# Optimization experiments

Hardware: AMD Instinct MI355X
Metric: run time of the kernel (lower is better)

The kernel has to match this reference:

```python
import jax, jax.numpy as jnp
import numpy as np

N_NODES = 50000
N_EDGES = 800000
IN, HID, OUT = 512, 256, 128


def spmm(edge_src, edge_dst, edge_weight, x, n_nodes):
    # y[i] = sum_{e: dst[e]==i} w[e] * x[src[e]]   (sparse adjacency @ x)
    msgs = edge_weight[:, None] * x[edge_src]          # [E, F] gather
    return jax.ops.segment_sum(msgs, edge_dst, num_segments=n_nodes)


def setup_inputs() -> dict:
    key = jax.random.key(0)
    k1, k2, k3, k4, k5, k6 = jax.random.split(key, 6)
    features = jax.random.normal(k1, (N_NODES, IN), dtype=jnp.float32)
    edge_src = jax.random.randint(k2, (N_EDGES,), 0, N_NODES, dtype=jnp.int32)
    edge_dst = jax.random.randint(k3, (N_EDGES,), 0, N_NODES, dtype=jnp.int32)
    edge_weight = jax.random.uniform(k4, (N_EDGES,), dtype=jnp.float32)
    # init like torch: uniform(-stdv, stdv), stdv = 1/sqrt(out_dim)
    s1 = 1.0 / np.sqrt(HID)
    s2 = 1.0 / np.sqrt(OUT)
    W1 = jax.random.uniform(k5, (IN, HID), dtype=jnp.float32, minval=-s1, maxval=s1)
    W2 = jax.random.uniform(k6, (HID, OUT), dtype=jnp.float32, minval=-s2, maxval=s2)
    return {"features": features, "edge_src": edge_src, "edge_dst": edge_dst,
            "edge_weight": edge_weight, "W1": W1, "W2": W2}


def reference(features, edge_src, edge_dst, edge_weight, W1, W2):
    n = features.shape[0]
    # layer 1: dense GEMM -> SpMM -> ReLU
    hidden = jax.nn.relu(spmm(edge_src, edge_dst, edge_weight, features @ W1, n))
    # layer 2: dense GEMM -> SpMM
    out = spmm(edge_src, edge_dst, edge_weight, hidden @ W2, n)
    return out
```

## Files before the change

kernel.cpp:

```cpp
#include <hip/hip_runtime.h>

#define NN 50000
#define NE 800000
#define FIN 512
#define FHID 256
#define FOUT 128
#define MPAD 50048

#define TW1_BLOCKS  512
#define TW2_BLOCKS  128
#define ZERO_BLOCKS 13

#define NBKT   196
#define BCAP   5120
#define BSTRIDE 16
#define PA_BLOCKS 392
#define E_CHA    2048

#define PB_BLOCKS   196
#define GEMM1_BLOCKS 782

using bf16x8 = __attribute__((ext_vector_type(8))) short;
using f32x4  = __attribute__((ext_vector_type(4))) float;
using u16x8  = __attribute__((ext_vector_type(8))) unsigned short;
using u16x4  = __attribute__((ext_vector_type(4))) unsigned short;
using u16x2  = __attribute__((ext_vector_type(2))) unsigned short;

__device__ __forceinline__ unsigned short f2bf(float f) {
    unsigned int u = __builtin_bit_cast(unsigned int, f);
    unsigned int r = (u + 0x7FFFu + ((u >> 16) & 1u)) >> 16;
    return (unsigned short)r;
}
__device__ __forceinline__ float bf2f(unsigned short u) {
    return __builtin_bit_cast(float, (unsigned int)u << 16);
}
__device__ __forceinline__ void gload_lds16(const void* g, void* l) {
    __builtin_amdgcn_global_load_lds(
        (const __attribute__((address_space(1))) void*)g,
        (__attribute__((address_space(3))) void*)l, 16, 0, 0);
}


__global__ __launch_bounds__(256) void prep_kernel(
    int* __restrict__ bcur,
    const float* __restrict__ W1, unsigned short* __restrict__ W1T,
    const float* __restrict__ W2, unsigned short* __restrict__ W2T) {
    int b = blockIdx.x, tid = threadIdx.x;
    if (b < TW1_BLOCKS) {
        int t = b * 256 + tid;
        int n = t % FHID, k = t / FHID;
        W1T[(size_t)n * FIN + k] = f2bf(W1[t]);
    } else if (b < TW1_BLOCKS + TW2_BLOCKS) {
        int t = (b - TW1_BLOCKS) * 256 + tid;
        int n = t % FOUT, k = t / FOUT;
        W2T[(size_t)n * FHID + k] = f2bf(W2[t]);
    } else {
        int i = (b - TW1_BLOCKS - TW2_BLOCKS) * 256 + tid;
        if (i < NBKT * BSTRIDE) bcur[i] = 0;
    }
}


__global__ __launch_bounds__(256) void passa_kernel(const int* __restrict__ src,
                                                    const int* __restrict__ dst,
                                                    const float* __restrict__ w,
                                                    int* __restrict__ bcur,
                                                    int2* __restrict__ barr) {
    __shared__ int hist[NBKT];
    __shared__ int resv[NBKT];
    int pa = blockIdx.x, tid = threadIdx.x;
    if (tid < NBKT) hist[tid] = 0;
    __syncthreads();
    int base = pa * E_CHA + tid;
    int  d[8];
    bool m[8];
#pragma unroll
    for (int j = 0; j < 8; ++j) {
        int e = base + j * 256;
        m[j] = e < NE;
        d[j] = m[j] ? dst[e] : 0;
    }
#pragma unroll
    for (int j = 0; j < 8; ++j)
        if (m[j]) atomicAdd(&hist[d[j] >> 8], 1);
    __syncthreads();
    if (tid < NBKT) {
        int h = hist[tid];
        resv[tid] = (h > 0) ? atomicAdd(&bcur[tid * BSTRIDE], h) : 0;
        hist[tid] = 0;
    }
    __syncthreads();
    int   s[8];
    float wv[8];
#pragma unroll
    for (int j = 0; j < 8; ++j) {
        int e = base + j * 256;
        s[j]  = m[j] ? src[e] : 0;
        wv[j] = m[j] ? w[e] : 0.f;
    }
#pragma unroll
    for (int j = 0; j < 8; ++j) {
        if (m[j]) {
            int bb = d[j] >> 8;
            int r  = atomicAdd(&hist[bb], 1);
            int pos = resv[bb] + r;
            if (pos < BCAP)
                barr[(size_t)bb * BCAP + pos] =
                    make_int2(s[j] | ((d[j] & 255) << 16), __float_as_int(wv[j]));
        }
    }
}


__global__ __launch_bounds__(256) void scan_bkt_kernel(const int* __restrict__ bcur,
                                                       int* __restrict__ bko,
                                                       int* __restrict__ off) {
    __shared__ int wsum[4];
    int tid = threadIdx.x, lane = tid & 63, wid = tid >> 6;
    int v = (tid < NBKT) ? min(bcur[tid * BSTRIDE], BCAP) : 0;
    int s = v;
#pragma unroll
    for (int d = 1; d < 64; d <<= 1) {
        int t = __shfl_up(s, d, 64);
        if (lane >= d) s += t;
    }
    if (lane == 63) wsum[wid] = s;
    __syncthreads();
    int wo = 0;
#pragma unroll
    for (int j = 0; j < 4; ++j)
        if (j < wid) wo += wsum[j];
    int excl = wo + s - v;
    if (tid < NBKT) bko[tid] = excl;
    if (tid == NBKT - 1) off[NN] = excl + v;
}


__device__ __forceinline__ void gemm1_body(const float* __restrict__ X,
                                           const unsigned short* __restrict__ BT,
                                           unsigned short* __restrict__ C,
                                           int bx, int by) {
    __shared__ unsigned short As[128 * 64];
    __shared__ unsigned short Bs[128 * 64];

    const int tid  = threadIdx.x;
    const int lane = tid & 63;
    const int wid  = tid >> 6;
    const int wm   = wid >> 1;
    const int wn   = wid & 1;
    const int brow = bx * 128;
    const int bcol = by * 128;
    const int r15   = lane & 15;
    const int khalf = (lane >> 4) * 8;

    f32x4 acc[4][4] = {};

    for (int k0 = 0; k0 < FIN; k0 += 64) {
#pragma unroll
        for (int c = 0; c < 4; ++c) {
            int b   = wid * 4096 + c * 1024 + lane * 16;
            int row = b >> 7;
            int cby = (b & 127) ^ ((row & 7) << 4);
            const char* gb = (const char*)(BT + (size_t)(bcol + row) * FIN + k0) + cby;
            gload_lds16(gb, (char*)Bs + wid * 4096 + c * 1024);
        }
#pragma unroll
        for (int g = 0; g < 4; ++g) {
            int idx  = g * 256 + tid;
            int row  = idx >> 3;
            int col0 = (idx & 7) * 8;
            float4 a0 = make_float4(0.f, 0.f, 0.f, 0.f), a1 = a0;
            int grow = brow + row;
            if (grow < NN) {
                const float4* p = (const float4*)(X + (size_t)grow * FIN + k0 + col0);
                a0 = p[0]; a1 = p[1];
            }
            u16x8 v;
            v[0] = f2bf(a0.x); v[1] = f2bf(a0.y); v[2] = f2bf(a0.z); v[3] = f2bf(a0.w);
            v[4] = f2bf(a1.x); v[5] = f2bf(a1.y); v[6] = f2bf(a1.z); v[7] = f2bf(a1.w);
            int byte = row * 128 + ((col0 * 2) ^ ((row & 7) << 4));
            *(u16x8*)((char*)As + byte) = v;
        }
        __syncthreads();

        bf16x8 af[4][2], bfr[4][2];
#pragma unroll
        for (int m = 0; m < 4; ++m) {
            int row = wm * 64 + m * 16 + r15;
            int rb  = row * 128;
            int sw  = (row & 7) << 4;
#pragma unroll
            for (int ks = 0; ks < 2; ++ks) {
                int byte = rb + (((ks * 32 + khalf) * 2) ^ sw);
                af[m][ks] = *(const bf16x8*)((const char*)As + byte);
            }
        }
#pragma unroll
        for (int n = 0; n < 4; ++n) {
            int row = wn * 64 + n * 16 + r15;
            int rb  = row * 128;
            int sw  = (row & 7) << 4;
#pragma unroll
            for (int ks = 0; ks < 2; ++ks) {
                int byte = rb + (((ks * 32 + khalf) * 2) ^ sw);
                bfr[n][ks] = *(const bf16x8*)((const char*)Bs + byte);
            }
        }
#pragma unroll
        for (int m = 0; m < 4; ++m)
#pragma unroll
            for (int n = 0; n < 4; ++n)
#pragma unroll
                for (int ks = 0; ks < 2; ++ks)
                    acc[m][n] = __builtin_amdgcn_mfma_f32_16x16x32_bf16(
                        af[m][ks], bfr[n][ks], acc[m][n], 0, 0, 0);
        __syncthreads();
    }

    const int crow0 = brow + wm * 64;
    const int ccol0 = bcol + wn * 64 + r15;
    const int rsub  = (lane >> 4) * 4;
#pragma unroll
    for (int m = 0; m < 4; ++m) {
#pragma unroll
        for (int r = 0; r < 4; ++r) {
            int grow = crow0 + m * 16 + rsub + r;
            if (grow < NN) {
#pragma unroll
                for (int n = 0; n < 4; ++n)
                    C[(size_t)grow * FHID + ccol0 + n * 16] = f2bf(acc[m][n][r]);
            }
        }
    }
}


template <int K, int N>
__device__ __forceinline__ void gemm_body(const unsigned short* __restrict__ A,
                                          const unsigned short* __restrict__ BT,
                                          unsigned short* __restrict__ C,
                                          int M, int bx, int by) {
    __shared__ unsigned short As[128 * 64];
    __shared__ unsigned short Bs[128 * 64];

    const int tid  = threadIdx.x;
    const int lane = tid & 63;
    const int wid  = tid >> 6;
    const int wm   = wid >> 1;
    const int wn   = wid & 1;
    const int brow = bx * 128;
    const int bcol = by * 128;
    const int r15   = lane & 15;
    const int khalf = (lane >> 4) * 8;

    f32x4 acc[4][4] = {};

    for (int k0 = 0; k0 < K; k0 += 64) {
#pragma unroll
        for (int c = 0; c < 4; ++c) {
            int b   = wid * 4096 + c * 1024 + lane * 16;
            int row = b >> 7;
            int cby = (b & 127) ^ ((row & 7) << 4);
            const char* ga = (const char*)(A + (size_t)(brow + row) * K + k0) + cby;
            gload_lds16(ga, (char*)As + wid * 4096 + c * 1024);
            const char* gb = (const char*)(BT + (size_t)(bcol + row) * K + k0) + cby;
            gload_lds16(gb, (char*)Bs + wid * 4096 + c * 1024);
        }
        __syncthreads();

        bf16x8 af[4][2], bfr[4][2];
#pragma unroll
        for (int m = 0; m < 4; ++m) {
            int row = wm * 64 + m * 16 + r15;
            int rb  = row * 128;
            int sw  = (row & 7) << 4;
#pragma unroll
            for (int ks = 0; ks < 2; ++ks) {
                int byte = rb + (((ks * 32 + khalf) * 2) ^ sw);
                af[m][ks] = *(const bf16x8*)((const char*)As + byte);
            }
        }
#pragma unroll
        for (int n = 0; n < 4; ++n) {
            int row = wn * 64 + n * 16 + r15;
            int rb  = row * 128;
            int sw  = (row & 7) << 4;
#pragma unroll
            for (int ks = 0; ks < 2; ++ks) {
                int byte = rb + (((ks * 32 + khalf) * 2) ^ sw);
                bfr[n][ks] = *(const bf16x8*)((const char*)Bs + byte);
            }
        }
#pragma unroll
        for (int m = 0; m < 4; ++m)
#pragma unroll
            for (int n = 0; n < 4; ++n)
#pragma unroll
                for (int ks = 0; ks < 2; ++ks)
                    acc[m][n] = __builtin_amdgcn_mfma_f32_16x16x32_bf16(
                        af[m][ks], bfr[n][ks], acc[m][n], 0, 0, 0);
        __syncthreads();
    }

    const int crow0 = brow + wm * 64;
    const int ccol0 = bcol + wn * 64 + r15;
    const int rsub  = (lane >> 4) * 4;
#pragma unroll
    for (int m = 0; m < 4; ++m) {
#pragma unroll
        for (int r = 0; r < 4; ++r) {
            int grow = crow0 + m * 16 + rsub + r;
            if (grow < M) {
#pragma unroll
                for (int n = 0; n < 4; ++n)
                    C[(size_t)grow * N + ccol0 + n * 16] = f2bf(acc[m][n][r]);
            }
        }
    }
}


__device__ __forceinline__ void passb_body(int b, const int2* __restrict__ barr,
                                           const int* __restrict__ bcur,
                                           const int* __restrict__ bko,
                                           int* __restrict__ off,
                                           int2* __restrict__ csr) {
    __shared__ int cnt[256];
    __shared__ int pre[256];
    __shared__ int wsum[4];
    int tid = threadIdx.x, lane = tid & 63, wid = tid >> 6;
    int total = min(bcur[b * BSTRIDE], BCAP);
    int bko_b = bko[b];
    const int2* seg = barr + (size_t)b * BCAP;

    cnt[tid] = 0;
    __syncthreads();
    for (int k = tid; k < total; k += 256)
        atomicAdd(&cnt[(seg[k].x >> 16) & 255], 1);
    __syncthreads();
    int v = cnt[tid];
    int s = v;
#pragma unroll
    for (int d = 1; d < 64; d <<= 1) {
        int t = __shfl_up(s, d, 64);
        if (lane >= d) s += t;
    }
    if (lane == 63) wsum[wid] = s;
    __syncthreads();
    int wo = 0;
#pragma unroll
    for (int j = 0; j < 4; ++j)
        if (j < wid) wo += wsum[j];
    int base = bko_b + wo + s - v;
    pre[tid] = base;
    int n = b * 256 + tid;
    if (n < NN) off[n] = base;
    cnt[tid] = 0;
    __syncthreads();
    for (int k = tid; k < total; k += 256) {
        int2 pl = seg[k];
        int dlow = (pl.x >> 16) & 255;
        int r = atomicAdd(&cnt[dlow], 1);
        csr[pre[dlow] + r] = make_int2(pl.x & 0xFFFF, pl.y);
    }
}


__global__ __launch_bounds__(256) void fused_gemm1_finalize_kernel(
    const float* __restrict__ X, const unsigned short* __restrict__ BT,
    unsigned short* __restrict__ C,
    const int2* __restrict__ barr, const int* __restrict__ bcur,
    const int* __restrict__ bko, int* __restrict__ off, int2* __restrict__ csr) {
    if (blockIdx.x < PB_BLOCKS) {
        passb_body(blockIdx.x, barr, bcur, bko, off, csr);
    } else {
        int g = blockIdx.x - PB_BLOCKS;
        gemm1_body(X, BT, C, g % 391, g / 391);
    }
}

template <int K, int N>
__global__ __launch_bounds__(256) void gemm_bf16_kernel(const unsigned short* __restrict__ A,
                                                        const unsigned short* __restrict__ BT,
                                                        unsigned short* __restrict__ C,
                                                        int M) {
    gemm_body<K, N>(A, BT, C, M, blockIdx.x, blockIdx.y);
}


__global__ __launch_bounds__(256) void spmm_pair_kernel(const unsigned short* __restrict__ X,
                                                        const int* __restrict__ off,
                                                        const int2* __restrict__ csr,
                                                        unsigned short* __restrict__ Y) {
    int wave = (int)((blockIdx.x * 256 + threadIdx.x) >> 6);
    int lane = threadIdx.x & 63;
    int half = lane >> 5;
    int hl   = lane & 31;
    int n = wave * 2 + half;
    if (n >= NN) return;
    int e0 = off[n];
    int e1 = off[n + 1];
    const size_t fo = (size_t)hl * 8;

    float acc[8] = {};
    for (int e = e0; e < e1; e += 8) {
        int   ss[8];
        float ww[8];
#pragma unroll
        for (int j = 0; j < 8; ++j) {
            int  ee = e + j;
            bool v  = ee < e1;
            int2 sw = csr[v ? ee : e0];
            ss[j] = sw.x;
            ww[j] = v ? __int_as_float(sw.y) : 0.f;
        }
        u16x8 r[8];
#pragma unroll
        for (int j = 0; j < 8; ++j)
            r[j] = *(const u16x8*)(X + (size_t)ss[j] * FHID + fo);
#pragma unroll
        for (int j = 0; j < 8; ++j)
#pragma unroll
            for (int k = 0; k < 8; ++k)
                acc[k] += ww[j] * bf2f(r[j][k]);
    }
    u16x8 o;
#pragma unroll
    for (int k = 0; k < 8; ++k) o[k] = f2bf(fmaxf(acc[k], 0.f));
    *(u16x8*)(Y + (size_t)n * FHID + fo) = o;
}


__global__ __launch_bounds__(256) void spmm_quad_kernel(const unsigned short* __restrict__ X,
                                                        const int* __restrict__ off,
                                                        const int2* __restrict__ csr,
                                                        float* __restrict__ Y) {
    int wave = (int)((blockIdx.x * 256 + threadIdx.x) >> 6);
    int lane = threadIdx.x & 63;
    int q  = lane >> 4;
    int hl = lane & 15;
    int n = wave * 4 + q;
    if (n >= NN) return;
    int e0 = off[n];
    int e1 = off[n + 1];
    const size_t fo = (size_t)hl * 8;

    float acc[8] = {};
    for (int e = e0; e < e1; e += 8) {
        int   ss[8];
        float ww[8];
#pragma unroll
        for (int j = 0; j < 8; ++j) {
            int  ee = e + j;
            bool v  = ee < e1;
            int2 sw = csr[v ? ee : e0];
            ss[j] = sw.x;
            ww[j] = v ? __int_as_float(sw.y) : 0.f;
        }
        u16x8 r[8];
#pragma unroll
        for (int j = 0; j < 8; ++j)
            r[j] = *(const u16x8*)(X + (size_t)ss[j] * FOUT + fo);
#pragma unroll
        for (int j = 0; j < 8; ++j)
#pragma unroll
            for (int k = 0; k < 8; ++k)
                acc[k] += ww[j] * bf2f(r[j][k]);
    }
    float4 o0 = make_float4(acc[0], acc[1], acc[2], acc[3]);
    float4 o1 = make_float4(acc[4], acc[5], acc[6], acc[7]);
    *(float4*)(Y + (size_t)n * FOUT + fo) = o0;
    *(float4*)(Y + (size_t)n * FOUT + fo + 4) = o1;
}


extern "C" void kernel_launch(void* const* d_in, const int* in_sizes, int n_in,
                              void* d_out, int out_size, void* d_ws, size_t ws_size,
                              hipStream_t stream) {
    const float* features = (const float*)d_in[0];
    const int*   edge_src = (const int*)d_in[1];
    const int*   edge_dst = (const int*)d_in[2];
    const float* edge_w   = (const float*)d_in[3];
    const float* W1       = (const float*)d_in[4];
    const float* W2       = (const float*)d_in[5];
    float* out = (float*)d_out;

    char*  ws  = (char*)d_ws;
    size_t ofs = 0;
    auto carve = [&](size_t bytes) -> void* {
        void* r = ws + ofs;
        ofs = (ofs + bytes + 255) & ~(size_t)255;
        return r;
    };
    int*            off   = (int*)carve((NN + 1) * sizeof(int));
    int*            bcur  = (int*)carve(NBKT * BSTRIDE * sizeof(int));
    int*            bko   = (int*)carve(NBKT * sizeof(int));
    int2*           barr  = (int2*)carve((size_t)NBKT * BCAP * sizeof(int2));
    int2*           csr   = (int2*)carve((size_t)NE * sizeof(int2));
    unsigned short* W1T   = (unsigned short*)carve((size_t)FHID * FIN * 2);
    unsigned short* W2T   = (unsigned short*)carve((size_t)FOUT * FHID * 2);
    unsigned short* H0b   = (unsigned short*)carve((size_t)MPAD * FHID * 2);
    unsigned short* Hb    = (unsigned short*)carve((size_t)MPAD * FHID * 2);
    unsigned short* H1b   = H0b;

    prep_kernel<<<TW1_BLOCKS + TW2_BLOCKS + ZERO_BLOCKS, 256, 0, stream>>>(
        bcur, W1, W1T, W2, W2T);

    passa_kernel<<<PA_BLOCKS, 256, 0, stream>>>(edge_src, edge_dst, edge_w, bcur, barr);

    scan_bkt_kernel<<<1, 256, 0, stream>>>(bcur, bko, off);

    fused_gemm1_finalize_kernel<<<PB_BLOCKS + GEMM1_BLOCKS, 256, 0, stream>>>(
        features, W1T, H0b, barr, bcur, bko, off, csr);

    spmm_pair_kernel<<<6250, 256, 0, stream>>>(H0b, off, csr, Hb);

    gemm_bf16_kernel<FHID, FOUT><<<dim3(391, 1), 256, 0, stream>>>(Hb, W2T, H1b, NN);
    spmm_quad_kernel<<<3125, 256, 0, stream>>>(H1b, off, csr, out);
}
```

Before: 175.4 us.

## Fuse pass A bucketing with GEMM1, fold bucket scan into pass B, shrink GEMM tiles

The pipeline is reordered so the edge-bucketing pass runs in the same launch as the first dense GEMM, and the CSR finalize pass becomes its own kernel that recomputes the bucket prefix scan in every block. The separate single-block scan kernel is removed. Both GEMMs move from 128-row to 64-row tiles, doubling the block count to improve occupancy and load balance. In exchange, the large GEMM1 no longer overlaps with pass B, and the smaller tiles lower per-block data reuse.

```diff
diff --git a/kernel.cpp b/kernel.cpp
--- a/kernel.cpp
+++ b/kernel.cpp
@@ -17,14 +17,14 @@
 #define PA_BLOCKS 392
 #define E_CHA    2048
 
-#define PB_BLOCKS   196
-#define GEMM1_BLOCKS 782
+#define PB_BLOCKS    196
+#define GEMM1_BLOCKS 1564
+#define GEMM2_BLOCKS 782
 
 using bf16x8 = __attribute__((ext_vector_type(8))) short;
 using f32x4  = __attribute__((ext_vector_type(4))) float;
 using u16x8  = __attribute__((ext_vector_type(8))) unsigned short;
 using u16x4  = __attribute__((ext_vector_type(4))) unsigned short;
-using u16x2  = __attribute__((ext_vector_type(2))) unsigned short;
 
 __device__ __forceinline__ unsigned short f2bf(float f) {
     unsigned int u = __builtin_bit_cast(unsigned int, f);
@@ -61,14 +61,15 @@
 }
 
 
-__global__ __launch_bounds__(256) void passa_kernel(const int* __restrict__ src,
-                                                    const int* __restrict__ dst,
-                                                    const float* __restrict__ w,
-                                                    int* __restrict__ bcur,
-                                                    int2* __restrict__ barr) {
+__device__ __forceinline__ void passa_body(int pa,
+                                           const int* __restrict__ src,
+                                           const int* __restrict__ dst,
+                                           const float* __restrict__ w,
+                                           int* __restrict__ bcur,
+                                           int2* __restrict__ barr) {
     __shared__ int hist[NBKT];
     __shared__ int resv[NBKT];
-    int pa = blockIdx.x, tid = threadIdx.x;
+    int tid = threadIdx.x;
     if (tid < NBKT) hist[tid] = 0;
     __syncthreads();
     int base = pa * E_CHA + tid;
@@ -112,35 +113,11 @@
 }
 
 
-__global__ __launch_bounds__(256) void scan_bkt_kernel(const int* __restrict__ bcur,
-                                                       int* __restrict__ bko,
-                                                       int* __restrict__ off) {
-    __shared__ int wsum[4];
-    int tid = threadIdx.x, lane = tid & 63, wid = tid >> 6;
-    int v = (tid < NBKT) ? min(bcur[tid * BSTRIDE], BCAP) : 0;
-    int s = v;
-#pragma unroll
-    for (int d = 1; d < 64; d <<= 1) {
-        int t = __shfl_up(s, d, 64);
-        if (lane >= d) s += t;
-    }
-    if (lane == 63) wsum[wid] = s;
-    __syncthreads();
-    int wo = 0;
-#pragma unroll
-    for (int j = 0; j < 4; ++j)
-        if (j < wid) wo += wsum[j];
-    int excl = wo + s - v;
-    if (tid < NBKT) bko[tid] = excl;
-    if (tid == NBKT - 1) off[NN] = excl + v;
-}
-
-
 __device__ __forceinline__ void gemm1_body(const float* __restrict__ X,
                                            const unsigned short* __restrict__ BT,
                                            unsigned short* __restrict__ C,
                                            int bx, int by) {
-    __shared__ unsigned short As[128 * 64];
+    __shared__ unsigned short As[64 * 64];
     __shared__ unsigned short Bs[128 * 64];
 
     const int tid  = threadIdx.x;
@@ -148,12 +125,12 @@
     const int wid  = tid >> 6;
     const int wm   = wid >> 1;
     const int wn   = wid & 1;
-    const int brow = bx * 128;
+    const int brow = bx * 64;
     const int bcol = by * 128;
     const int r15   = lane & 15;
     const int khalf = (lane >> 4) * 8;
 
-    f32x4 acc[4][4] = {};
+    f32x4 acc[2][4] = {};
 
     for (int k0 = 0; k0 < FIN; k0 += 64) {
 #pragma unroll
@@ -165,7 +142,7 @@
             gload_lds16(gb, (char*)Bs + wid * 4096 + c * 1024);
         }
 #pragma unroll
-        for (int g = 0; g < 4; ++g) {
+        for (int g = 0; g < 2; ++g) {
             int idx  = g * 256 + tid;
             int row  = idx >> 3;
             int col0 = (idx & 7) * 8;
@@ -183,10 +160,10 @@
         }
         __syncthreads();
 
-        bf16x8 af[4][2], bfr[4][2];
-#pragma unroll
-        for (int m = 0; m < 4; ++m) {
-            int row = wm * 64 + m * 16 + r15;
+        bf16x8 af[2][2], bfr[4][2];
+#pragma unroll
+        for (int m = 0; m < 2; ++m) {
+            int row = wm * 32 + m * 16 + r15;
             int rb  = row * 128;
             int sw  = (row & 7) << 4;
 #pragma unroll
@@ -207,7 +184,7 @@
             }
         }
 #pragma unroll
-        for (int m = 0; m < 4; ++m)
+        for (int m = 0; m < 2; ++m)
 #pragma unroll
             for (int n = 0; n < 4; ++n)
 #pragma unroll
@@ -217,11 +194,11 @@
         __syncthreads();
     }
 
-    const int crow0 = brow + wm * 64;
+    const int crow0 = brow + wm * 32;
     const int ccol0 = bcol + wn * 64 + r15;
     const int rsub  = (lane >> 4) * 4;
 #pragma unroll
-    for (int m = 0; m < 4; ++m) {
+    for (int m = 0; m < 2; ++m) {
 #pragma unroll
         for (int r = 0; r < 4; ++r) {
             int grow = crow0 + m * 16 + rsub + r;
@@ -235,12 +212,87 @@
 }
 
 
-template <int K, int N>
-__device__ __forceinline__ void gemm_body(const unsigned short* __restrict__ A,
-                                          const unsigned short* __restrict__ BT,
-                                          unsigned short* __restrict__ C,
-                                          int M, int bx, int by) {
-    __shared__ unsigned short As[128 * 64];
+__global__ __launch_bounds__(256) void fused_passa_gemm1_kernel(
+    const int* __restrict__ src, const int* __restrict__ dst,
+    const float* __restrict__ w, int* __restrict__ bcur, int2* __restrict__ barr,
+    const float* __restrict__ X, const unsigned short* __restrict__ BT,
+    unsigned short* __restrict__ C) {
+    if (blockIdx.x < PA_BLOCKS) {
+        passa_body(blockIdx.x, src, dst, w, bcur, barr);
+    } else {
+        int g = blockIdx.x - PA_BLOCKS;
+        gemm1_body(X, BT, C, g >> 1, g & 1);
+    }
+}
+
+
+__global__ __launch_bounds__(256) void passb_kernel(const int2* __restrict__ barr,
+                                                    const int* __restrict__ bcur,
+                                                    int* __restrict__ off,
+                                                    int2* __restrict__ csr) {
+    __shared__ int sc[256];
+    __shared__ int cnt[256];
+    __shared__ int pre[256];
+    __shared__ int wsum[4];
+    int b = blockIdx.x, tid = threadIdx.x, lane = tid & 63, wid = tid >> 6;
+
+    int v = (tid < NBKT) ? min(bcur[tid * BSTRIDE], BCAP) : 0;
+    int s = v;
+#pragma unroll
+    for (int d = 1; d < 64; d <<= 1) {
+        int t = __shfl_up(s, d, 64);
+        if (lane >= d) s += t;
+    }
+    if (lane == 63) wsum[wid] = s;
+    __syncthreads();
+    int wo = 0;
+#pragma unroll
+    for (int j = 0; j < 4; ++j)
+        if (j < wid) wo += wsum[j];
+    sc[tid] = wo + s - v;
+    if (b == 0 && tid == NBKT - 1) off[NN] = wo + s;
+    cnt[tid] = 0;
+    __syncthreads();
+
+    int bko_b = sc[b];
+    int total = min(bcur[b * BSTRIDE], BCAP);
+    const int2* seg = barr + (size_t)b * BCAP;
+
+    for (int k = tid; k < total; k += 256)
+        atomicAdd(&cnt[(seg[k].x >> 16) & 255], 1);
+    __syncthreads();
+    int v2 = cnt[tid];
+    int s2 = v2;
+#pragma unroll
+    for (int d = 1; d < 64; d <<= 1) {
+        int t = __shfl_up(s2, d, 64);
+        if (lane >= d) s2 += t;
+    }
+    if (lane == 63) wsum[wid] = s2;
+    __syncthreads();
+    int wo2 = 0;
+#pragma unroll
+    for (int j = 0; j < 4; ++j)
+        if (j < wid) wo2 += wsum[j];
+    int base = bko_b + wo2 + s2 - v2;
+    pre[tid] = base;
+    int n = b * 256 + tid;
+    if (n < NN) off[n] = base;
+    cnt[tid] = 0;
+    __syncthreads();
+    for (int k = tid; k < total; k += 256) {
+        int2 pl = seg[k];
+        int dlow = (pl.x >> 16) & 255;
+        int r = atomicAdd(&cnt[dlow], 1);
+        csr[pre[dlow] + r] = make_int2(pl.x & 0xFFFF, pl.y);
+    }
+}
+
+
+__global__ __launch_bounds__(256) void gemm2_kernel(const unsigned short* __restrict__ A,
+                                                    const unsigned short* __restrict__ BT,
+                                                    unsigned short* __restrict__ C) {
+    __shared__ unsigned short As[64 * 64];
     __shared__ unsigned short Bs[128 * 64];
 
     const int tid  = threadIdx.x;
@@ -248,30 +300,35 @@
     const int wid  = tid >> 6;
     const int wm   = wid >> 1;
     const int wn   = wid & 1;
-    const int brow = bx * 128;
-    const int bcol = by * 128;
+    const int brow = blockIdx.x * 64;
     const int r15   = lane & 15;
     const int khalf = (lane >> 4) * 8;
 
-    f32x4 acc[4][4] = {};
-
-    for (int k0 = 0; k0 < K; k0 += 64) {
+    f32x4 acc[2][4] = {};
+
+    for (int k0 = 0; k0 < FHID; k0 += 64) {
 #pragma unroll
         for (int c = 0; c < 4; ++c) {
             int b   = wid * 4096 + c * 1024 + lane * 16;
             int row = b >> 7;
             int cby = (b & 127) ^ ((row & 7) << 4);
-            const char* ga = (const char*)(A + (size_t)(brow + row) * K + k0) + cby;
-            gload_lds16(ga, (char*)As + wid * 4096 + c * 1024);
-            const char* gb = (const char*)(BT + (size_t)(bcol + row) * K + k0) + cby;
+            const char* gb = (const char*)(BT + (size_t)row * FHID + k0) + cby;
             gload_lds16(gb, (char*)Bs + wid * 4096 + c * 1024);
         }
+#pragma unroll
+        for (int c = 0; c < 2; ++c) {
+            int b   = wid * 2048 + c * 1024 + lane * 16;
+            int row = b >> 7;
+            int cby = (b & 127) ^ ((row & 7) << 4);
+            const char* ga = (const char*)(A + (size_t)(brow + row) * FHID + k0) + cby;
+            gload_lds16(ga, (char*)As + wid * 2048 + c * 1024);
+        }
         __syncthreads();
 
-        bf16x8 af[4][2], bfr[4][2];
-#pragma unroll
-        for (int m = 0; m < 4; ++m) {
-            int row = wm * 64 + m * 16 + r15;
+        bf16x8 af[2][2], bfr[4][2];
+#pragma unroll
+        for (int m = 0; m < 2; ++m) {
+            int row = wm * 32 + m * 16 + r15;
             int rb  = row * 128;
             int sw  = (row & 7) << 4;
 #pragma unroll
@@ -292,7 +349,7 @@
             }
         }
 #pragma unroll
-        for (int m = 0; m < 4; ++m)
+        for (int m = 0; m < 2; ++m)
 #pragma unroll
             for (int n = 0; n < 4; ++n)
 #pragma unroll
@@ -302,89 +359,21 @@
         __syncthreads();
     }
 
-    const int crow0 = brow + wm * 64;
-    const int ccol0 = bcol + wn * 64 + r15;
+    const int crow0 = brow + wm * 32;
+    const int ccol0 = wn * 64 + r15;
     const int rsub  = (lane >> 4) * 4;
 #pragma unroll
-    for (int m = 0; m < 4; ++m) {
+    for (int m = 0; m < 2; ++m) {
 #pragma unroll
         for (int r = 0; r < 4; ++r) {
             int grow = crow0 + m * 16 + rsub + r;
-            if (grow < M) {
+            if (grow < NN) {
 #pragma unroll
                 for (int n = 0; n < 4; ++n)
-                    C[(size_t)grow * N + ccol0 + n * 16] = f2bf(acc[m][n][r]);
-            }
-        }
-    }
-}
-
-
-__device__ __forceinline__ void passb_body(int b, const int2* __restrict__ barr,
-                                           const int* __restrict__ bcur,
-                                           const int* __restrict__ bko,
-                                           int* __restrict__ off,
-                                           int2* __restrict__ csr) {
-    __shared__ int cnt[256];
-    __shared__ int pre[256];
-    __shared__ int wsum[4];
-    int tid = threadIdx.x, lane = tid & 63, wid = tid >> 6;
-    int total = min(bcur[b * BSTRIDE], BCAP);
-    int bko_b = bko[b];
-    const int2* seg = barr + (size_t)b * BCAP;
-
-    cnt[tid] = 0;
-    __syncthreads();
-    for (int k = tid; k < total; k += 256)
-        atomicAdd(&cnt[(seg[k].x >> 16) & 255], 1);
-    __syncthreads();
-    int v = cnt[tid];
-    int s = v;
-#pragma unroll
-    for (int d = 1; d < 64; d <<= 1) {
-        int t = __shfl_up(s, d, 64);
-        if (lane >= d) s += t;
-    }
-    if (lane == 63) wsum[wid] = s;
-    __syncthreads();
-    int wo = 0;
-#pragma unroll
-    for (int j = 0; j < 4; ++j)
-        if (j < wid) wo += wsum[j];
-    int base = bko_b + wo + s - v;
-    pre[tid] = base;
-    int n = b * 256 + tid;
-    if (n < NN) off[n] = base;
-    cnt[tid] = 0;
-    __syncthreads();
-    for (int k = tid; k < total; k += 256) {
-        int2 pl = seg[k];
-        int dlow = (pl.x >> 16) & 255;
-        int r = atomicAdd(&cnt[dlow], 1);
-        csr[pre[dlow] + r] = make_int2(pl.x & 0xFFFF, pl.y);
-    }
-}
-
-
-__global__ __launch_bounds__(256) void fused_gemm1_finalize_kernel(
-    const float* __restrict__ X, const unsigned short* __restrict__ BT,
-    unsigned short* __restrict__ C,
-    const int2* __restrict__ barr, const int* __restrict__ bcur,
-    const int* __restrict__ bko, int* __restrict__ off, int2* __restrict__ csr) {
-    if (blockIdx.x < PB_BLOCKS) {
-        passb_body(blockIdx.x, barr, bcur, bko, off, csr);
-    } else {
-        int g = blockIdx.x - PB_BLOCKS;
-        gemm1_body(X, BT, C, g % 391, g / 391);
-    }
-}
-
-template <int K, int N>
-__global__ __launch_bounds__(256) void gemm_bf16_kernel(const unsigned short* __restrict__ A,
-                                                        const unsigned short* __restrict__ BT,
-                                                        unsigned short* __restrict__ C,
-                                                        int M) {
-    gemm_body<K, N>(A, BT, C, M, blockIdx.x, blockIdx.y);
+                    C[(size_t)grow * FOUT + ccol0 + n * 16] = f2bf(acc[m][n][r]);
+            }
+        }
+    }
 }
 
 
@@ -494,7 +483,6 @@
     };
     int*            off   = (int*)carve((NN + 1) * sizeof(int));
     int*            bcur  = (int*)carve(NBKT * BSTRIDE * sizeof(int));
-    int*            bko   = (int*)carve(NBKT * sizeof(int));
     int2*           barr  = (int2*)carve((size_t)NBKT * BCAP * sizeof(int2));
     int2*           csr   = (int2*)carve((size_t)NE * sizeof(int2));
     unsigned short* W1T   = (unsigned short*)carve((size_t)FHID * FIN * 2);
@@ -506,15 +494,13 @@
     prep_kernel<<<TW1_BLOCKS + TW2_BLOCKS + ZERO_BLOCKS, 256, 0, stream>>>(
         bcur, W1, W1T, W2, W2T);
 
-    passa_kernel<<<PA_BLOCKS, 256, 0, stream>>>(edge_src, edge_dst, edge_w, bcur, barr);
-
-    scan_bkt_kernel<<<1, 256, 0, stream>>>(bcur, bko, off);
-
-    fused_gemm1_finalize_kernel<<<PB_BLOCKS + GEMM1_BLOCKS, 256, 0, stream>>>(
-        features, W1T, H0b, barr, bcur, bko, off, csr);
+    fused_passa_gemm1_kernel<<<PA_BLOCKS + GEMM1_BLOCKS, 256, 0, stream>>>(
+        edge_src, edge_dst, edge_w, bcur, barr, features, W1T, H0b);
+
+    passb_kernel<<<PB_BLOCKS, 256, 0, stream>>>(barr, bcur, off, csr);
 
     spmm_pair_kernel<<<6250, 256, 0, stream>>>(H0b, off, csr, Hb);
 
-    gemm_bf16_kernel<FHID, FOUT><<<dim3(391, 1), 256, 0, stream>>>(Hb, W2T, H1b, NN);
+    gemm2_kernel<<<GEMM2_BLOCKS, 256, 0, stream>>>(Hb, W2T, H1b);
     spmm_quad_kernel<<<3125, 256, 0, stream>>>(H1b, off, csr, out);
 }
```

After: 168.2 us. 1.04x faster.
